# Kernel optimization log

Hardware: AMD Instinct MI355X
Metric: run time of the kernel (lower is better)

The kernel has to match this reference:

```python
import jax, jax.numpy as jnp
import numpy as np

N = 131072          # events
N_OBS = 64          # observables
HID = [512, 512, 512]          # trunk hidden widths
SUB_HID = [512, 256]           # per-pair subnetwork hidden widths
P = 3                          # number of pairings


def _glorot(key, shape):
    fan_in, fan_out = shape[-2], shape[-1]
    lim = np.sqrt(6.0 / (fan_in + fan_out)).astype(np.float32)
    return jax.random.uniform(key, shape, jnp.float32, -lim, lim)


def setup_inputs() -> dict:
    key = jax.random.key(0)
    ks = jax.random.split(key, 16)
    x = jax.random.normal(ks[0], (N, N_OBS), jnp.float32)
    y = jax.random.randint(ks[1], (N,), 0, 3)
    pairs = jnp.array([[0, 1], [0, 2], [1, 2]], dtype=jnp.int32)
    # trunk params
    W0 = _glorot(ks[2], (N_OBS, HID[0])); b0 = jnp.zeros((HID[0],), jnp.float32)
    W1 = _glorot(ks[3], (HID[0], HID[1])); b1 = jnp.zeros((HID[1],), jnp.float32)
    W2 = _glorot(ks[4], (HID[1], HID[2])); b2 = jnp.zeros((HID[2],), jnp.float32)
    # stacked per-pair subnetwork params (all P subnets share shapes)
    SW0 = _glorot(ks[5], (P, HID[2], SUB_HID[0])); Sb0 = jnp.zeros((P, SUB_HID[0]), jnp.float32)
    SW1 = _glorot(ks[6], (P, SUB_HID[0], SUB_HID[1])); Sb1 = jnp.zeros((P, SUB_HID[1]), jnp.float32)
    SW2 = _glorot(ks[7], (P, SUB_HID[1], 1)); Sb2 = jnp.zeros((P, 1), jnp.float32)
    return {"x": x, "y": y, "pairs": pairs,
            "W0": W0, "b0": b0, "W1": W1, "b1": b1, "W2": W2, "b2": b2,
            "SW0": SW0, "Sb0": Sb0, "SW1": SW1, "Sb1": Sb1, "SW2": SW2, "Sb2": Sb2}


def reference(x, y, pairs, W0, b0, W1, b1, W2, b2, SW0, Sb0, SW1, Sb1, SW2, Sb2):
    relu = jax.nn.relu
    # Trunk. Note: in the torch module with dropout_prob>0, the first Linear sits at
    # layer index 1, so the activation is applied to the raw input as well (eval-mode
    # dropout == identity). We reproduce that exactly.
    h = relu(x) @ W0 + b0
    h = relu(h) @ W1 + b1
    repr_ = relu(h) @ W2 + b2                      # [N, HID[-1]]

    # Per-pair membership masks (jit-safe stand-in for the variable-size gather):
    # mask[p, n] = True iff y[n] is one of the two labels of pairing p.
    mask = (y[None, :] == pairs[:, 0:1]) | (y[None, :] == pairs[:, 1:2])  # [P, N] bool

    # Per-pair RatioModel subnetworks, batched over the pair dim.
    # Same activation-before-every-Linear pattern as the trunk (dropout indices).
    hs = jnp.einsum('nd,pdh->pnh', relu(repr_), SW0) + Sb0[:, None, :]
    hs = jnp.einsum('pnh,phk->pnk', relu(hs), SW1) + Sb1[:, None, :]
    logit = jnp.einsum('pnk,pko->pno', relu(hs), SW2) + Sb2[:, None, :]  # [P, N, 1]
    s_hat = jnp.clip(jax.nn.sigmoid(logit[..., 0]), 1e-9, None)          # [P, N]
    r_hat = (1.0 - s_hat) / s_hat                                        # [P, N]

    maskf = mask.astype(s_hat.dtype)
    return repr_, r_hat * maskf, s_hat * maskf, mask
```

## Files before the change

kernel.cpp:

```cpp
#include <hip/hip_runtime.h>
#include <hip/hip_bf16.h>
#include <stdint.h>

#define NE 131072
#define CHUNK 32768

typedef __attribute__((ext_vector_type(8))) short bf16x8;
typedef __attribute__((ext_vector_type(4))) float f32x4;

__device__ __forceinline__ unsigned short f2bf(float f) {
  unsigned u = __float_as_uint(f);
  u += 0x7FFF + ((u >> 16) & 1);
  return (unsigned short)(u >> 16);
}
__device__ __forceinline__ float bf2f(unsigned short h) {
  return __uint_as_float((unsigned)h << 16);
}

__device__ __forceinline__ void gload_lds16(const void* g, void* l) {
  __builtin_amdgcn_global_load_lds(
      (const __attribute__((address_space(1))) unsigned*)g,
      (__attribute__((address_space(3))) unsigned*)l, 16, 0, 0);
}

__global__ void transpose_cvt(const float* __restrict__ src,
                              unsigned short* __restrict__ dst,
                              int K, int Nc) {
  int p = blockIdx.y;
  long base = (long)p * K * Nc;
  int tot = K * Nc;
  for (int i = blockIdx.x * blockDim.x + threadIdx.x; i < tot;
       i += gridDim.x * blockDim.x) {
    int n = i / K, k = i - n * K;
    dst[base + i] = f2bf(src[base + (long)k * Nc + n]);
  }
}

__global__ void relu_cvt_x(const float4* __restrict__ x,
                           ushort4* __restrict__ xb) {
  int i = blockIdx.x * blockDim.x + threadIdx.x;
  float4 v = x[i];
  ushort4 o;
  o.x = f2bf(fmaxf(v.x, 0.f));
  o.y = f2bf(fmaxf(v.y, 0.f));
  o.z = f2bf(fmaxf(v.z, 0.f));
  o.w = f2bf(fmaxf(v.w, 0.f));
  xb[i] = o;
}

__global__ __launch_bounds__(256, 2) void gemm_bf16(
    const unsigned short* __restrict__ A, long aZ,
    const unsigned short* __restrict__ Bt, long bZ,
    const float* __restrict__ bias, long biasZ,
    float* __restrict__ outF,
    unsigned short* __restrict__ outA, long cZ,
    int K, int Nc) {
  __shared__ unsigned short As[128 * 32];
  __shared__ unsigned short Bs[128 * 32];
  const int z = blockIdx.z;
  A += (long)z * aZ;
  Bt += (long)z * bZ;
  bias += (long)z * biasZ;
  if (outF) outF += (long)z * cZ;
  if (outA) outA += (long)z * cZ;

  const int tid = threadIdx.x;
  const int wave = tid >> 6, lane = tid & 63;
  const int wr = wave >> 1, wc = wave & 1;
  const int lr = lane & 15, lh = lane >> 4;
  const long row0 = (long)blockIdx.x * 128;
  const int col0 = blockIdx.y * 128;

  f32x4 acc[4][4];
#pragma unroll
  for (int m = 0; m < 4; ++m)
#pragma unroll
    for (int n = 0; n < 4; ++n) acc[m][n] = (f32x4){0.f, 0.f, 0.f, 0.f};

  const int nk = K >> 5;
  for (int kt = 0; kt < nk; ++kt) {
    const int k0 = kt << 5;
#pragma unroll
    for (int i = 0; i < 2; ++i) {
      int c = i * 256 + wave * 64 + lane;
      int r = c >> 2, k8 = (c & 3) * 8;
      gload_lds16(A + (row0 + r) * K + k0 + k8, &As[(i * 256 + wave * 64) * 8]);
      gload_lds16(Bt + (long)(col0 + r) * K + k0 + k8,
                  &Bs[(i * 256 + wave * 64) * 8]);
    }
    __syncthreads();
    bf16x8 af[4], bfr[4];
#pragma unroll
    for (int m = 0; m < 4; ++m)
      af[m] = *(const bf16x8*)&As[(wr * 64 + m * 16 + lr) * 32 + lh * 8];
#pragma unroll
    for (int n = 0; n < 4; ++n)
      bfr[n] = *(const bf16x8*)&Bs[(wc * 64 + n * 16 + lr) * 32 + lh * 8];
#pragma unroll
    for (int m = 0; m < 4; ++m)
#pragma unroll
      for (int n = 0; n < 4; ++n)
        acc[m][n] =
            __builtin_amdgcn_mfma_f32_16x16x32_bf16(af[m], bfr[n], acc[m][n], 0, 0, 0);
    __syncthreads();
  }

  float bv[4];
#pragma unroll
  for (int n = 0; n < 4; ++n) bv[n] = bias[col0 + wc * 64 + n * 16 + lr];
#pragma unroll
  for (int m = 0; m < 4; ++m) {
    long rbase = row0 + wr * 64 + m * 16 + lh * 4;
#pragma unroll
    for (int r = 0; r < 4; ++r) {
      long rr = rbase + r;
#pragma unroll
      for (int n = 0; n < 4; ++n) {
        int cc = col0 + wc * 64 + n * 16 + lr;
        float v = acc[m][n][r] + bv[n];
        if (outF) outF[rr * Nc + cc] = v;
        if (outA) outA[rr * Nc + cc] = f2bf(fmaxf(v, 0.f));
      }
    }
  }
}

__global__ __launch_bounds__(512) void gemm_sw1_head(
    const unsigned short* __restrict__ A3,
    const unsigned short* __restrict__ SW1t,
    const float* __restrict__ Sb1,
    const unsigned short* __restrict__ W2b,
    const float* __restrict__ Sb2,
    const int* __restrict__ y,
    const int* __restrict__ pairs,
    int r0,
    float* __restrict__ outR, float* __restrict__ outS,
    float* __restrict__ outM) {
  __shared__ unsigned short As[128 * 32];
  __shared__ unsigned short Bs[256 * 32];
  __shared__ float part[4][128];

  const int p = blockIdx.z;
  const unsigned short* A = A3 + (long)p * CHUNK * 512;
  const unsigned short* Bt = SW1t + (long)p * 256 * 512;
  const float* bias = Sb1 + p * 256;
  const unsigned short* w2 = W2b + p * 256;

  const int tid = threadIdx.x;
  const int wave = tid >> 6, lane = tid & 63;
  const int wr = wave >> 2, wc = wave & 3;
  const int lr = lane & 15, lh = lane >> 4;
  const long row0 = (long)blockIdx.x * 128;

  f32x4 acc[4][4];
#pragma unroll
  for (int m = 0; m < 4; ++m)
#pragma unroll
    for (int n = 0; n < 4; ++n) acc[m][n] = (f32x4){0.f, 0.f, 0.f, 0.f};

  for (int kt = 0; kt < 16; ++kt) {
    const int k0 = kt << 5;
    gload_lds16(A + (row0 + (tid >> 2)) * 512 + k0 + (tid & 3) * 8,
                &As[wave * 64 * 8]);
#pragma unroll
    for (int i = 0; i < 2; ++i) {
      int c = i * 512 + tid;
      int r = c >> 2, k8 = (c & 3) * 8;
      gload_lds16(Bt + (long)r * 512 + k0 + k8, &Bs[(i * 512 + wave * 64) * 8]);
    }
    __syncthreads();
    bf16x8 af[4], bfr[4];
#pragma unroll
    for (int m = 0; m < 4; ++m)
      af[m] = *(const bf16x8*)&As[(wr * 64 + m * 16 + lr) * 32 + lh * 8];
#pragma unroll
    for (int n = 0; n < 4; ++n)
      bfr[n] = *(const bf16x8*)&Bs[(wc * 64 + n * 16 + lr) * 32 + lh * 8];
#pragma unroll
    for (int m = 0; m < 4; ++m)
#pragma unroll
      for (int n = 0; n < 4; ++n)
        acc[m][n] =
            __builtin_amdgcn_mfma_f32_16x16x32_bf16(af[m], bfr[n], acc[m][n], 0, 0, 0);
    __syncthreads();
  }

  float bv[4], w2v[4];
#pragma unroll
  for (int n = 0; n < 4; ++n) {
    int cc = wc * 64 + n * 16 + lr;
    bv[n] = bias[cc];
    w2v[n] = bf2f(w2[cc]);
  }
#pragma unroll
  for (int m = 0; m < 4; ++m) {
#pragma unroll
    for (int r = 0; r < 4; ++r) {
      float s = 0.f;
#pragma unroll
      for (int n = 0; n < 4; ++n) {
        float v = fmaxf(acc[m][n][r] + bv[n], 0.f);
        s += v * w2v[n];
      }
#pragma unroll
      for (int off = 1; off < 16; off <<= 1) s += __shfl_xor(s, off);
      if (lr == 0) part[wc][wr * 64 + m * 16 + lh * 4 + r] = s;
    }
  }
  __syncthreads();
  if (tid < 128) {
    float logit = part[0][tid] + part[1][tid] + part[2][tid] + part[3][tid] +
                  Sb2[p];
    float s = 1.f / (1.f + expf(-logit));
    s = fmaxf(s, 1e-9f);
    float r = (1.f - s) / s;
    long n = (long)r0 + row0 + tid;
    int yv = y[n];
    float mf = (yv == pairs[p * 2] || yv == pairs[p * 2 + 1]) ? 1.f : 0.f;
    outR[(long)p * NE + n] = r * mf;
    outS[(long)p * NE + n] = s * mf;
    outM[(long)p * NE + n] = mf;
  }
}

extern "C" void kernel_launch(void* const* d_in, const int* in_sizes, int n_in,
                              void* d_out, int out_size, void* d_ws, size_t ws_size,
                              hipStream_t stream) {
  const float* x   = (const float*)d_in[0];
  const int*   y   = (const int*)d_in[1];
  const int*   prs = (const int*)d_in[2];
  const float* W0  = (const float*)d_in[3];
  const float* b0  = (const float*)d_in[4];
  const float* W1  = (const float*)d_in[5];
  const float* b1  = (const float*)d_in[6];
  const float* W2  = (const float*)d_in[7];
  const float* b2  = (const float*)d_in[8];
  const float* SW0 = (const float*)d_in[9];
  const float* Sb0 = (const float*)d_in[10];
  const float* SW1 = (const float*)d_in[11];
  const float* Sb1 = (const float*)d_in[12];
  const float* SW2 = (const float*)d_in[13];
  const float* Sb2 = (const float*)d_in[14];

  uint8_t* ws = (uint8_t*)d_ws;
  size_t off = 0;
  auto take = [&](size_t bytes) -> void* {
    void* ptr = ws + off;
    off = (off + bytes + 255) & ~(size_t)255;
    return ptr;
  };
  unsigned short* W0t  = (unsigned short*)take((size_t)64 * 512 * 2);
  unsigned short* W1t  = (unsigned short*)take((size_t)512 * 512 * 2);
  unsigned short* W2t  = (unsigned short*)take((size_t)512 * 512 * 2);
  unsigned short* SW0t = (unsigned short*)take((size_t)3 * 512 * 512 * 2);
  unsigned short* SW1t = (unsigned short*)take((size_t)3 * 256 * 512 * 2);
  unsigned short* SW2b = (unsigned short*)take((size_t)3 * 256 * 2);
  unsigned short* Xb   = (unsigned short*)take((size_t)NE * 64 * 2);
  unsigned short* A3   = (unsigned short*)take((size_t)3 * CHUNK * 512 * 2);
  unsigned short* T0   = A3;
  unsigned short* T1   = A3 + (size_t)CHUNK * 512;
  unsigned short* bufR = (unsigned short*)take((size_t)CHUNK * 512 * 2);

  float* out   = (float*)d_out;
  float* outRe = out;
  float* outR  = out + (size_t)NE * 512;
  float* outS  = outR + (size_t)3 * NE;
  float* outM  = outS + (size_t)3 * NE;

  transpose_cvt<<<dim3(128, 1), 256, 0, stream>>>(W0, W0t, 64, 512);
  transpose_cvt<<<dim3(1024, 1), 256, 0, stream>>>(W1, W1t, 512, 512);
  transpose_cvt<<<dim3(1024, 1), 256, 0, stream>>>(W2, W2t, 512, 512);
  transpose_cvt<<<dim3(1024, 3), 256, 0, stream>>>(SW0, SW0t, 512, 512);
  transpose_cvt<<<dim3(512, 3), 256, 0, stream>>>(SW1, SW1t, 512, 256);
  transpose_cvt<<<dim3(1, 3), 256, 0, stream>>>(SW2, SW2b, 256, 1);
  relu_cvt_x<<<dim3(NE * 64 / 4 / 256), 256, 0, stream>>>((const float4*)x,
                                                          (ushort4*)Xb);

  for (int c = 0; c < NE / CHUNK; ++c) {
    size_t r0 = (size_t)c * CHUNK;
    gemm_bf16<<<dim3(CHUNK / 128, 4, 1), 256, 0, stream>>>(
        Xb + r0 * 64, 0, W0t, 0, b0, 0, nullptr, T0, 0, 64, 512);
    gemm_bf16<<<dim3(CHUNK / 128, 4, 1), 256, 0, stream>>>(
        T0, 0, W1t, 0, b1, 0, nullptr, T1, 0, 512, 512);
    gemm_bf16<<<dim3(CHUNK / 128, 4, 1), 256, 0, stream>>>(
        T1, 0, W2t, 0, b2, 0, outRe + r0 * 512, bufR, 0, 512, 512);
    gemm_bf16<<<dim3(CHUNK / 128, 4, 3), 256, 0, stream>>>(
        bufR, 0, SW0t, (long)512 * 512, Sb0, 512, nullptr, A3,
        (long)CHUNK * 512, 512, 512);
    gemm_sw1_head<<<dim3(CHUNK / 128, 1, 3), 512, 0, stream>>>(
        A3, SW1t, Sb1, SW2b, Sb2, y, prs, (int)r0, outR, outS, outM);
  }
}
```

Baseline: 767.0 us.

## Use 256x256 tiled GEMM with multi-stage async LDS pipeline and swizzle

Replaces the 128x128 single-buffered GEMM for the 512-wide layers and the SW1 head with a new 256x256-tile, 8-wave kernel. It uses K=64 double-buffered LDS tiles filled by direct global-to-LDS loads, staged in quarters interleaved with MFMA groups. The kernel also adds an XOR swizzle against bank conflicts, s_setprio around MFMA bursts, and fine-grained vmcnt waits. The goal is higher reuse per loaded tile and overlap of memory traffic with matrix math. In exchange it uses 128KB LDS and many accumulators per block, which limits occupancy, and the fused head epilogue now covers 256 rows per block.

New measurement: 802.7 us. +4.7%, slower.

```diff
diff --git a/kernel.cpp b/kernel.cpp
--- a/kernel.cpp
+++ b/kernel.cpp
@@ -49,21 +49,13 @@
 }
 
 __global__ __launch_bounds__(256, 2) void gemm_bf16(
-    const unsigned short* __restrict__ A, long aZ,
-    const unsigned short* __restrict__ Bt, long bZ,
-    const float* __restrict__ bias, long biasZ,
-    float* __restrict__ outF,
-    unsigned short* __restrict__ outA, long cZ,
+    const unsigned short* __restrict__ A,
+    const unsigned short* __restrict__ Bt,
+    const float* __restrict__ bias,
+    unsigned short* __restrict__ outA,
     int K, int Nc) {
   __shared__ unsigned short As[128 * 32];
   __shared__ unsigned short Bs[128 * 32];
-  const int z = blockIdx.z;
-  A += (long)z * aZ;
-  Bt += (long)z * bZ;
-  bias += (long)z * biasZ;
-  if (outF) outF += (long)z * cZ;
-  if (outA) outA += (long)z * cZ;
-
   const int tid = threadIdx.x;
   const int wave = tid >> 6, lane = tid & 63;
   const int wr = wave >> 1, wc = wave & 1;
@@ -118,108 +110,190 @@
       for (int n = 0; n < 4; ++n) {
         int cc = col0 + wc * 64 + n * 16 + lr;
         float v = acc[m][n][r] + bv[n];
-        if (outF) outF[rr * Nc + cc] = v;
-        if (outA) outA[rr * Nc + cc] = f2bf(fmaxf(v, 0.f));
+        outA[rr * Nc + cc] = f2bf(fmaxf(v, 0.f));
       }
     }
   }
 }
 
-__global__ __launch_bounds__(512) void gemm_sw1_head(
-    const unsigned short* __restrict__ A3,
-    const unsigned short* __restrict__ SW1t,
-    const float* __restrict__ Sb1,
+#define MFMA16(MQ, N0)                                                       \
+  _Pragma("unroll") for (int m = 0; m < 4; ++m)                              \
+  _Pragma("unroll") for (int n = 0; n < 2; ++n)                              \
+  _Pragma("unroll") for (int kk = 0; kk < 2; ++kk)                           \
+      acc[(MQ)*4 + m][(N0) + n] = __builtin_amdgcn_mfma_f32_16x16x32_bf16(   \
+          a[m][kk], b[(N0) + n][kk], acc[(MQ)*4 + m][(N0) + n], 0, 0, 0);
+
+__global__ __launch_bounds__(512) void gemm256(
+    const unsigned short* __restrict__ A, long aZ,
+    const unsigned short* __restrict__ Bt, long bZ,
+    const float* __restrict__ bias, long biasZ,
+    float* __restrict__ outF,
+    unsigned short* __restrict__ outA, long cZ,
+    int K, int Nc,
     const unsigned short* __restrict__ W2b,
-    const float* __restrict__ Sb2,
-    const int* __restrict__ y,
-    const int* __restrict__ pairs,
-    int r0,
+    const float* __restrict__ Sb2, const int* __restrict__ y,
+    const int* __restrict__ pairs, int r0,
     float* __restrict__ outR, float* __restrict__ outS,
     float* __restrict__ outM) {
-  __shared__ unsigned short As[128 * 32];
-  __shared__ unsigned short Bs[256 * 32];
-  __shared__ float part[4][128];
-
-  const int p = blockIdx.z;
-  const unsigned short* A = A3 + (long)p * CHUNK * 512;
-  const unsigned short* Bt = SW1t + (long)p * 256 * 512;
-  const float* bias = Sb1 + p * 256;
-  const unsigned short* w2 = W2b + p * 256;
+  __shared__ unsigned short lds[65536];
+  const int z = blockIdx.z;
+  A += (long)z * aZ;
+  Bt += (long)z * bZ;
+  bias += (long)z * biasZ;
+  if (outA) outA += (long)z * cZ;
 
   const int tid = threadIdx.x;
   const int wave = tid >> 6, lane = tid & 63;
-  const int wr = wave >> 2, wc = wave & 3;
+  const int wm = wave >> 2, wn = wave & 3;
   const int lr = lane & 15, lh = lane >> 4;
-  const long row0 = (long)blockIdx.x * 128;
-
-  f32x4 acc[4][4];
-#pragma unroll
-  for (int m = 0; m < 4; ++m)
+  const long brow = (long)blockIdx.x * 256;
+  const int bcol = blockIdx.y * 256;
+  const int nk = K >> 6;
+
+  const int lsrc = lane ^ (((lane >> 5) & 1) << 1);
+  const int srow = lsrc >> 3;
+  const int skel = (lsrc & 7) * 8;
+  const int acol = (lh * 8) ^ (((lr >> 2) & 1) << 4);
+
+  f32x4 acc[8][4];
+#pragma unroll
+  for (int m = 0; m < 8; ++m)
 #pragma unroll
     for (int n = 0; n < 4; ++n) acc[m][n] = (f32x4){0.f, 0.f, 0.f, 0.f};
 
-  for (int kt = 0; kt < 16; ++kt) {
-    const int k0 = kt << 5;
-    gload_lds16(A + (row0 + (tid >> 2)) * 512 + k0 + (tid & 3) * 8,
-                &As[wave * 64 * 8]);
+  auto STAGE = [&](int S) {
+    if (S >= nk * 4) return;
+    const int tile = S >> 2, slot = S & 3, buf = tile & 1, half = slot & 1;
+    const int k0 = tile << 6;
+    const unsigned short* src;
+    long rb;
+    int lbase;
+    if (slot >= 2) {
+      src = A;  rb = brow + half * 128;  lbase = buf * 16384 + half * 8192;
+    } else {
+      src = Bt; rb = bcol + half * 128;  lbase = 32768 + buf * 16384 + half * 8192;
+    }
 #pragma unroll
     for (int i = 0; i < 2; ++i) {
-      int c = i * 512 + tid;
-      int r = c >> 2, k8 = (c & 3) * 8;
-      gload_lds16(Bt + (long)r * 512 + k0 + k8, &Bs[(i * 512 + wave * 64) * 8]);
-    }
+      int c = wave * 2 + i;
+      gload_lds16(src + (rb + c * 8 + srow) * K + k0 + skel,
+                  &lds[lbase + c * 512]);
+    }
+  };
+
+#pragma unroll
+  for (int S0 = 0; S0 < 7; ++S0) STAGE(S0);
+  asm volatile("s_waitcnt vmcnt(6)" ::: "memory");
+  __builtin_amdgcn_s_barrier();
+
+  bf16x8 a[4][2], b[4][2];
+  int S = 7;
+  for (int t = 0; t < nk; ++t) {
+    const int buf = t & 1;
+    const int ab = buf * 16384 + wm * 8192;
+    const int bb = 32768 + buf * 16384 + (wn >> 1) * 8192 + (wn & 1) * 64 * 64;
+#pragma unroll
+    for (int m = 0; m < 4; ++m) {
+      a[m][0] = *(const bf16x8*)&lds[ab + (m * 16 + lr) * 64 + acol];
+      a[m][1] = *(const bf16x8*)&lds[ab + (m * 16 + lr) * 64 + 32 + acol];
+    }
+#pragma unroll
+    for (int n = 0; n < 4; ++n) {
+      b[n][0] = *(const bf16x8*)&lds[bb + (n * 16 + lr) * 64 + acol];
+      b[n][1] = *(const bf16x8*)&lds[bb + (n * 16 + lr) * 64 + 32 + acol];
+    }
+    STAGE(S++);
+    __builtin_amdgcn_s_barrier();
+    __builtin_amdgcn_s_setprio(1);
+    MFMA16(0, 0)
+    __builtin_amdgcn_s_setprio(0);
+    __builtin_amdgcn_s_barrier();
+    STAGE(S++);
+    __builtin_amdgcn_s_barrier();
+    __builtin_amdgcn_s_setprio(1);
+    MFMA16(0, 2)
+    __builtin_amdgcn_s_setprio(0);
+    __builtin_amdgcn_s_barrier();
+#pragma unroll
+    for (int m = 0; m < 4; ++m) {
+      a[m][0] = *(const bf16x8*)&lds[ab + ((m + 4) * 16 + lr) * 64 + acol];
+      a[m][1] = *(const bf16x8*)&lds[ab + ((m + 4) * 16 + lr) * 64 + 32 + acol];
+    }
+    STAGE(S++);
+    __builtin_amdgcn_s_barrier();
+    __builtin_amdgcn_s_setprio(1);
+    MFMA16(1, 2)
+    __builtin_amdgcn_s_setprio(0);
+    __builtin_amdgcn_s_barrier();
+    STAGE(S++);
+    if (t < nk - 2)
+      asm volatile("s_waitcnt vmcnt(6)" ::: "memory");
+    else
+      asm volatile("s_waitcnt vmcnt(0)" ::: "memory");
+    __builtin_amdgcn_s_barrier();
+    __builtin_amdgcn_s_setprio(1);
+    MFMA16(1, 0)
+    __builtin_amdgcn_s_setprio(0);
+    __builtin_amdgcn_s_barrier();
+  }
+
+  if (!W2b) {
+    float bv[4];
+#pragma unroll
+    for (int n = 0; n < 4; ++n) bv[n] = bias[bcol + wn * 64 + n * 16 + lr];
+#pragma unroll
+    for (int m = 0; m < 8; ++m) {
+      long rbase = brow + wm * 128 + m * 16 + lh * 4;
+#pragma unroll
+      for (int r = 0; r < 4; ++r) {
+        long rr = rbase + r;
+#pragma unroll
+        for (int n = 0; n < 4; ++n) {
+          int cc = bcol + wn * 64 + n * 16 + lr;
+          float v = acc[m][n][r] + bv[n];
+          if (outF) outF[rr * Nc + cc] = v;
+          if (outA) outA[rr * Nc + cc] = f2bf(fmaxf(v, 0.f));
+        }
+      }
+    }
+  } else {
+    const unsigned short* w2 = W2b + z * 256;
+    float bv[4], w2v[4];
+#pragma unroll
+    for (int n = 0; n < 4; ++n) {
+      int cc = wn * 64 + n * 16 + lr;
+      bv[n] = bias[cc];
+      w2v[n] = bf2f(w2[cc]);
+    }
+    float* part = (float*)lds;
     __syncthreads();
-    bf16x8 af[4], bfr[4];
-#pragma unroll
-    for (int m = 0; m < 4; ++m)
-      af[m] = *(const bf16x8*)&As[(wr * 64 + m * 16 + lr) * 32 + lh * 8];
-#pragma unroll
-    for (int n = 0; n < 4; ++n)
-      bfr[n] = *(const bf16x8*)&Bs[(wc * 64 + n * 16 + lr) * 32 + lh * 8];
-#pragma unroll
-    for (int m = 0; m < 4; ++m)
-#pragma unroll
-      for (int n = 0; n < 4; ++n)
-        acc[m][n] =
-            __builtin_amdgcn_mfma_f32_16x16x32_bf16(af[m], bfr[n], acc[m][n], 0, 0, 0);
+#pragma unroll
+    for (int m = 0; m < 8; ++m) {
+#pragma unroll
+      for (int r = 0; r < 4; ++r) {
+        float s = 0.f;
+#pragma unroll
+        for (int n = 0; n < 4; ++n)
+          s += fmaxf(acc[m][n][r] + bv[n], 0.f) * w2v[n];
+#pragma unroll
+        for (int off = 1; off < 16; off <<= 1) s += __shfl_xor(s, off);
+        if (lr == 0) part[wn * 256 + wm * 128 + m * 16 + lh * 4 + r] = s;
+      }
+    }
     __syncthreads();
-  }
-
-  float bv[4], w2v[4];
-#pragma unroll
-  for (int n = 0; n < 4; ++n) {
-    int cc = wc * 64 + n * 16 + lr;
-    bv[n] = bias[cc];
-    w2v[n] = bf2f(w2[cc]);
-  }
-#pragma unroll
-  for (int m = 0; m < 4; ++m) {
-#pragma unroll
-    for (int r = 0; r < 4; ++r) {
-      float s = 0.f;
-#pragma unroll
-      for (int n = 0; n < 4; ++n) {
-        float v = fmaxf(acc[m][n][r] + bv[n], 0.f);
-        s += v * w2v[n];
-      }
-#pragma unroll
-      for (int off = 1; off < 16; off <<= 1) s += __shfl_xor(s, off);
-      if (lr == 0) part[wc][wr * 64 + m * 16 + lh * 4 + r] = s;
-    }
-  }
-  __syncthreads();
-  if (tid < 128) {
-    float logit = part[0][tid] + part[1][tid] + part[2][tid] + part[3][tid] +
-                  Sb2[p];
-    float s = 1.f / (1.f + expf(-logit));
-    s = fmaxf(s, 1e-9f);
-    float r = (1.f - s) / s;
-    long n = (long)r0 + row0 + tid;
-    int yv = y[n];
-    float mf = (yv == pairs[p * 2] || yv == pairs[p * 2 + 1]) ? 1.f : 0.f;
-    outR[(long)p * NE + n] = r * mf;
-    outS[(long)p * NE + n] = s * mf;
-    outM[(long)p * NE + n] = mf;
+    if (tid < 256) {
+      float logit = part[tid] + part[256 + tid] + part[512 + tid] +
+                    part[768 + tid] + Sb2[z];
+      float s = 1.f / (1.f + expf(-logit));
+      s = fmaxf(s, 1e-9f);
+      float rr = (1.f - s) / s;
+      long n = (long)r0 + brow + tid;
+      int yv = y[n];
+      float mf = (yv == pairs[z * 2] || yv == pairs[z * 2 + 1]) ? 1.f : 0.f;
+      outR[(long)z * NE + n] = rr * mf;
+      outS[(long)z * NE + n] = s * mf;
+      outM[(long)z * NE + n] = mf;
+    }
   }
 }
 
@@ -278,16 +352,21 @@
 
   for (int c = 0; c < NE / CHUNK; ++c) {
     size_t r0 = (size_t)c * CHUNK;
-    gemm_bf16<<<dim3(CHUNK / 128, 4, 1), 256, 0, stream>>>(
-        Xb + r0 * 64, 0, W0t, 0, b0, 0, nullptr, T0, 0, 64, 512);
-    gemm_bf16<<<dim3(CHUNK / 128, 4, 1), 256, 0, stream>>>(
-        T0, 0, W1t, 0, b1, 0, nullptr, T1, 0, 512, 512);
-    gemm_bf16<<<dim3(CHUNK / 128, 4, 1), 256, 0, stream>>>(
-        T1, 0, W2t, 0, b2, 0, outRe + r0 * 512, bufR, 0, 512, 512);
-    gemm_bf16<<<dim3(CHUNK / 128, 4, 3), 256, 0, stream>>>(
+    gemm_bf16<<<dim3(CHUNK / 128, 4), 256, 0, stream>>>(Xb + r0 * 64, W0t, b0,
+                                                        T0, 64, 512);
+    gemm256<<<dim3(CHUNK / 256, 2, 1), 512, 0, stream>>>(
+        T0, 0, W1t, 0, b1, 0, nullptr, T1, 0, 512, 512,
+        nullptr, nullptr, nullptr, nullptr, 0, nullptr, nullptr, nullptr);
+    gemm256<<<dim3(CHUNK / 256, 2, 1), 512, 0, stream>>>(
+        T1, 0, W2t, 0, b2, 0, outRe + r0 * 512, bufR, 0, 512, 512,
+        nullptr, nullptr, nullptr, nullptr, 0, nullptr, nullptr, nullptr);
+    gemm256<<<dim3(CHUNK / 256, 2, 3), 512, 0, stream>>>(
         bufR, 0, SW0t, (long)512 * 512, Sb0, 512, nullptr, A3,
-        (long)CHUNK * 512, 512, 512);
-    gemm_sw1_head<<<dim3(CHUNK / 128, 1, 3), 512, 0, stream>>>(
-        A3, SW1t, Sb1, SW2b, Sb2, y, prs, (int)r0, outR, outS, outM);
-  }
-}
+        (long)CHUNK * 512, 512, 512,
+        nullptr, nullptr, nullptr, nullptr, 0, nullptr, nullptr, nullptr);
+    gemm256<<<dim3(CHUNK / 256, 1, 3), 512, 0, stream>>>(
+        A3, (long)CHUNK * 512, SW1t, (long)256 * 512, Sb1, 256, nullptr,
+        nullptr, 0, 512, 256,
+        SW2b, Sb2, y, prs, (int)r0, outR, outS, outM);
+  }
+}
```
